# Optimization experiments

Hardware: AMD Instinct MI355X
Metric: run time of the kernel (lower is better)

The kernel has to match this reference:

```python
import jax, jax.numpy as jnp
import numpy as np

POOL_SIZE = 4
MAX_DIM = 256
GRID = MAX_DIM // POOL_SIZE  # 64
NUM_CELLS = GRID * GRID      # 4096
B = 64                        # static max_batch (batch.max()+1 in torch)
N = 1_000_000
C = 64


def setup_inputs() -> dict:
    key = jax.random.key(0)
    k1, k2, k3 = jax.random.split(key, 3)
    x = jax.random.normal(k1, (N, C), dtype=jnp.float32)
    pos = jax.random.randint(k2, (N, 2), 0, MAX_DIM, dtype=jnp.int64)
    batch = jnp.sort(jax.random.randint(k3, (N,), 0, B, dtype=jnp.int64))
    return {"x": x, "pos": pos, "batch": batch}


def reference(x, pos, batch):
    # voxel key: (batch, pos_x//pool, pos_y//pool) -> flat cell index
    qpos = pos[:, :2] // POOL_SIZE                       # [N, 2] int
    idx = batch * NUM_CELLS + qpos[:, 0] * GRID + qpos[:, 1]  # [N]
    num_seg = B * NUM_CELLS
    # scatter_reduce(amax, include_self=False): max over points in each cell
    pooled = jax.ops.segment_max(x, idx, num_segments=num_seg)  # empty -> -inf
    # cells with no points stay zero (output_x initialized to zeros in torch)
    counts = jax.ops.segment_sum(jnp.ones((x.shape[0], 1), x.dtype), idx,
                                 num_segments=num_seg)          # [num_seg, 1]
    pooled = jnp.where(counts > 0, pooled, jnp.zeros((), x.dtype))
    # [B, grid^2, C] -> flatten -> [B, grid^2 * C]
    return pooled.reshape(B, NUM_CELLS * x.shape[1])
```

## Files before the change

kernel.cpp:

```cpp
#include <hip/hip_runtime.h>

#define POOL_SHIFT 2
#define GRID_DIM 64
#define NUM_CELLS 4096
#define NCH 64
#define BATCH 64
#define NSEG (BATCH * NUM_CELLS)
#define SCAN_BLOCKS 1024

__global__ __launch_bounds__(256) void count_kernel(
    const int* __restrict__ pos, const int* __restrict__ batch,
    unsigned int* __restrict__ counts, unsigned int* __restrict__ rank,
    int* __restrict__ cell, int n) {
    int p = blockIdx.x * blockDim.x + threadIdx.x;
    if (p >= n) return;
    int2 pp = ((const int2*)pos)[p];
    int c = batch[p] * NUM_CELLS + (pp.x >> POOL_SHIFT) * GRID_DIM + (pp.y >> POOL_SHIFT);
    cell[p] = c;
    rank[p] = atomicAdd(&counts[c], 1u);
}

__global__ __launch_bounds__(256) void reduce_kernel(
    const unsigned int* __restrict__ counts, unsigned int* __restrict__ blocksum) {
    __shared__ unsigned int s[256];
    int t = threadIdx.x;
    s[t] = counts[blockIdx.x * 256 + t];
    __syncthreads();
    for (int off = 128; off > 0; off >>= 1) {
        if (t < off) s[t] += s[t + off];
        __syncthreads();
    }
    if (t == 0) blocksum[blockIdx.x] = s[0];
}

__global__ __launch_bounds__(1024) void scanblock_kernel(
    const unsigned int* __restrict__ blocksum, unsigned int* __restrict__ blockbase) {
    __shared__ unsigned int s[1024];
    int t = threadIdx.x;
    unsigned int own = blocksum[t];
    s[t] = own;
    __syncthreads();
    for (int off = 1; off < 1024; off <<= 1) {
        unsigned int v = (t >= off) ? s[t - off] : 0u;
        __syncthreads();
        s[t] += v;
        __syncthreads();
    }
    blockbase[t] = s[t] - own;
}

__global__ __launch_bounds__(256) void offsets_kernel(
    const unsigned int* __restrict__ counts, const unsigned int* __restrict__ blockbase,
    unsigned int* __restrict__ offsets, int n) {
    __shared__ unsigned int s[256];
    int t = threadIdx.x, b = blockIdx.x;
    unsigned int own = counts[b * 256 + t];
    s[t] = own;
    __syncthreads();
    for (int off = 1; off < 256; off <<= 1) {
        unsigned int v = (t >= off) ? s[t - off] : 0u;
        __syncthreads();
        s[t] += v;
        __syncthreads();
    }
    unsigned int incl = s[t] + blockbase[b];
    offsets[b * 256 + t] = incl - own;
    if (b == SCAN_BLOCKS - 1 && t == 255) offsets[NSEG] = incl;
}

__global__ __launch_bounds__(256) void reorder_kernel(
    const int* __restrict__ cell, const unsigned int* __restrict__ rank,
    const unsigned int* __restrict__ offsets, unsigned int* __restrict__ order, int n) {
    int p = blockIdx.x * blockDim.x + threadIdx.x;
    if (p >= n) return;
    int c = cell[p];
    order[offsets[c] + rank[p]] = (unsigned int)p;
}

__global__ __launch_bounds__(256) void gather_kernel(
    const float* __restrict__ x, const unsigned int* __restrict__ offsets,
    const unsigned int* __restrict__ order, float* __restrict__ out) {
    int wave = (int)((blockIdx.x * blockDim.x + threadIdx.x) >> 6);
    int lane = threadIdx.x & 63;
    unsigned int s = offsets[wave];
    unsigned int e = offsets[wave + 1];

    size_t obase = (size_t)wave * NCH + lane;
    if (s == e) { out[obase] = 0.0f; return; }

    const float NEG_INF = -__builtin_inff();
    float acc = NEG_INF;

    for (unsigned int base = s; base < e; base += 64) {
        unsigned int rem = e - base;
        unsigned int cnt = rem < 64u ? rem : 64u;
        unsigned int li = lane < cnt ? (unsigned int)lane : cnt - 1u;
        unsigned int myp = order[base + li];

        for (unsigned int j = 0; j < cnt; j += 4) {
            unsigned int m = cnt - j;
            unsigned int p0 = (unsigned int)__shfl((int)myp, (int)j, 64);
            float v0 = x[(size_t)p0 * NCH + lane];
            float v1 = NEG_INF, v2 = NEG_INF, v3 = NEG_INF;
            if (m > 1u) {
                unsigned int p1 = (unsigned int)__shfl((int)myp, (int)(j + 1), 64);
                v1 = x[(size_t)p1 * NCH + lane];
            }
            if (m > 2u) {
                unsigned int p2 = (unsigned int)__shfl((int)myp, (int)(j + 2), 64);
                v2 = x[(size_t)p2 * NCH + lane];
            }
            if (m > 3u) {
                unsigned int p3 = (unsigned int)__shfl((int)myp, (int)(j + 3), 64);
                v3 = x[(size_t)p3 * NCH + lane];
            }
            acc = fmaxf(acc, fmaxf(fmaxf(v0, v1), fmaxf(v2, v3)));
        }
    }
    out[obase] = acc;
}

extern "C" void kernel_launch(void* const* d_in, const int* in_sizes, int n_in,
                              void* d_out, int out_size, void* d_ws, size_t ws_size,
                              hipStream_t stream) {
    const float* x   = (const float*)d_in[0];
    const int* pos   = (const int*)d_in[1];
    const int* batch = (const int*)d_in[2];
    float* out = (float*)d_out;
    int n = in_sizes[2];

    unsigned int* counts    = (unsigned int*)d_ws;
    unsigned int* offsets   = counts + NSEG;
    unsigned int* blocksum  = offsets + NSEG + 1;
    unsigned int* blockbase = blocksum + 1024;
    unsigned int* rank      = blockbase + 1024;
    int*          cell      = (int*)(rank + n);
    unsigned int* order     = (unsigned int*)(cell + n);

    hipMemsetAsync(counts, 0, (size_t)NSEG * sizeof(unsigned int), stream);

    int pblocks = (n + 255) / 256;
    count_kernel<<<pblocks, 256, 0, stream>>>(pos, batch, counts, rank, cell, n);
    reduce_kernel<<<SCAN_BLOCKS, 256, 0, stream>>>(counts, blocksum);
    scanblock_kernel<<<1, 1024, 0, stream>>>(blocksum, blockbase);
    offsets_kernel<<<SCAN_BLOCKS, 256, 0, stream>>>(counts, blockbase, offsets, n);
    reorder_kernel<<<pblocks, 256, 0, stream>>>(cell, rank, offsets, order, n);
    gather_kernel<<<NSEG / 4, 256, 0, stream>>>(x, offsets, order, out);
}
```

Baseline: 445.4 us.

## Pack cell and rank, use wave-shuffle scans, grid-stride loops and nontemporal accesses

Packs the cell index and the per-cell rank into one 32-bit word, so the count and reorder kernels write and read a single array instead of two. Replaces the shared-memory tree reduce and scans with wave-level shuffle reductions and scans. Converts the point and gather kernels to grid-stride loops with fixed grid sizes, and adds nontemporal loads and stores on the streaming x reads and output writes. The packing caps the rank at 14 bits (16384 points per cell), which holds for the expected densities but would silently corrupt results if a cell overflows.

```diff
diff --git a/kernel.cpp b/kernel.cpp
--- a/kernel.cpp
+++ b/kernel.cpp
@@ -7,117 +7,129 @@
 #define BATCH 64
 #define NSEG (BATCH * NUM_CELLS)
 #define SCAN_BLOCKS 1024
+#define RANK_BITS 14
+#define RANK_MASK ((1u << RANK_BITS) - 1u)
 
 __global__ __launch_bounds__(256) void count_kernel(
     const int* __restrict__ pos, const int* __restrict__ batch,
-    unsigned int* __restrict__ counts, unsigned int* __restrict__ rank,
-    int* __restrict__ cell, int n) {
-    int p = blockIdx.x * blockDim.x + threadIdx.x;
-    if (p >= n) return;
-    int2 pp = ((const int2*)pos)[p];
-    int c = batch[p] * NUM_CELLS + (pp.x >> POOL_SHIFT) * GRID_DIM + (pp.y >> POOL_SHIFT);
-    cell[p] = c;
-    rank[p] = atomicAdd(&counts[c], 1u);
+    unsigned int* __restrict__ counts, unsigned int* __restrict__ cellrank, int n) {
+    int stride = gridDim.x * blockDim.x;
+    for (int p = blockIdx.x * blockDim.x + threadIdx.x; p < n; p += stride) {
+        long long t = __builtin_nontemporal_load((const long long*)pos + p);
+        int px = (int)t;
+        int py = (int)(t >> 32);
+        int b  = __builtin_nontemporal_load(&batch[p]);
+        int c  = b * NUM_CELLS + (px >> POOL_SHIFT) * GRID_DIM + (py >> POOL_SHIFT);
+        unsigned int r = atomicAdd(&counts[c], 1u);
+        __builtin_nontemporal_store(((unsigned int)c << RANK_BITS) | r, &cellrank[p]);
+    }
 }
 
 __global__ __launch_bounds__(256) void reduce_kernel(
     const unsigned int* __restrict__ counts, unsigned int* __restrict__ blocksum) {
-    __shared__ unsigned int s[256];
+    __shared__ unsigned int ws[4];
     int t = threadIdx.x;
-    s[t] = counts[blockIdx.x * 256 + t];
+    unsigned int v = counts[blockIdx.x * 256 + t];
+    #pragma unroll
+    for (int off = 1; off < 64; off <<= 1) v += __shfl_xor((int)v, off, 64);
+    if ((t & 63) == 0) ws[t >> 6] = v;
     __syncthreads();
-    for (int off = 128; off > 0; off >>= 1) {
-        if (t < off) s[t] += s[t + off];
-        __syncthreads();
-    }
-    if (t == 0) blocksum[blockIdx.x] = s[0];
+    if (t == 0) blocksum[blockIdx.x] = ws[0] + ws[1] + ws[2] + ws[3];
 }
 
 __global__ __launch_bounds__(1024) void scanblock_kernel(
     const unsigned int* __restrict__ blocksum, unsigned int* __restrict__ blockbase) {
-    __shared__ unsigned int s[1024];
-    int t = threadIdx.x;
+    __shared__ unsigned int wsum[16];
+    int t = threadIdx.x, lane = t & 63, w = t >> 6;
     unsigned int own = blocksum[t];
-    s[t] = own;
+    unsigned int v = own;
+    #pragma unroll
+    for (int off = 1; off < 64; off <<= 1) {
+        unsigned int u = __shfl_up((int)v, off, 64);
+        if (lane >= off) v += u;
+    }
+    if (lane == 63) wsum[w] = v;
     __syncthreads();
-    for (int off = 1; off < 1024; off <<= 1) {
-        unsigned int v = (t >= off) ? s[t - off] : 0u;
-        __syncthreads();
-        s[t] += v;
-        __syncthreads();
-    }
-    blockbase[t] = s[t] - own;
+    unsigned int base = 0;
+    for (int i = 0; i < w; ++i) base += wsum[i];
+    blockbase[t] = v + base - own;
 }
 
 __global__ __launch_bounds__(256) void offsets_kernel(
     const unsigned int* __restrict__ counts, const unsigned int* __restrict__ blockbase,
     unsigned int* __restrict__ offsets, int n) {
-    __shared__ unsigned int s[256];
-    int t = threadIdx.x, b = blockIdx.x;
+    __shared__ unsigned int wsum[4];
+    int t = threadIdx.x, b = blockIdx.x, lane = t & 63, w = t >> 6;
     unsigned int own = counts[b * 256 + t];
-    s[t] = own;
+    unsigned int v = own;
+    #pragma unroll
+    for (int off = 1; off < 64; off <<= 1) {
+        unsigned int u = __shfl_up((int)v, off, 64);
+        if (lane >= off) v += u;
+    }
+    if (lane == 63) wsum[w] = v;
     __syncthreads();
-    for (int off = 1; off < 256; off <<= 1) {
-        unsigned int v = (t >= off) ? s[t - off] : 0u;
-        __syncthreads();
-        s[t] += v;
-        __syncthreads();
-    }
-    unsigned int incl = s[t] + blockbase[b];
+    unsigned int base = blockbase[b];
+    for (int i = 0; i < w; ++i) base += wsum[i];
+    unsigned int incl = v + base;
     offsets[b * 256 + t] = incl - own;
     if (b == SCAN_BLOCKS - 1 && t == 255) offsets[NSEG] = incl;
 }
 
 __global__ __launch_bounds__(256) void reorder_kernel(
-    const int* __restrict__ cell, const unsigned int* __restrict__ rank,
+    const unsigned int* __restrict__ cellrank,
     const unsigned int* __restrict__ offsets, unsigned int* __restrict__ order, int n) {
-    int p = blockIdx.x * blockDim.x + threadIdx.x;
-    if (p >= n) return;
-    int c = cell[p];
-    order[offsets[c] + rank[p]] = (unsigned int)p;
+    int stride = gridDim.x * blockDim.x;
+    for (int p = blockIdx.x * blockDim.x + threadIdx.x; p < n; p += stride) {
+        unsigned int u = __builtin_nontemporal_load(&cellrank[p]);
+        unsigned int c = u >> RANK_BITS;
+        order[offsets[c] + (u & RANK_MASK)] = (unsigned int)p;
+    }
 }
 
 __global__ __launch_bounds__(256) void gather_kernel(
     const float* __restrict__ x, const unsigned int* __restrict__ offsets,
     const unsigned int* __restrict__ order, float* __restrict__ out) {
-    int wave = (int)((blockIdx.x * blockDim.x + threadIdx.x) >> 6);
     int lane = threadIdx.x & 63;
-    unsigned int s = offsets[wave];
-    unsigned int e = offsets[wave + 1];
+    int gw = (int)((blockIdx.x * blockDim.x + threadIdx.x) >> 6);
+    int nw = (int)((gridDim.x * blockDim.x) >> 6);
+    const float NEG_INF = -__builtin_inff();
 
-    size_t obase = (size_t)wave * NCH + lane;
-    if (s == e) { out[obase] = 0.0f; return; }
+    for (int cell = gw; cell < NSEG; cell += nw) {
+        unsigned int s = offsets[cell];
+        unsigned int e = offsets[cell + 1];
+        size_t obase = (size_t)cell * NCH + lane;
+        if (s == e) { __builtin_nontemporal_store(0.0f, &out[obase]); continue; }
 
-    const float NEG_INF = -__builtin_inff();
-    float acc = NEG_INF;
+        float acc = NEG_INF;
+        for (unsigned int base = s; base < e; base += 64) {
+            unsigned int rem = e - base;
+            unsigned int cnt = rem < 64u ? rem : 64u;
+            unsigned int li = (unsigned int)lane < cnt ? (unsigned int)lane : cnt - 1u;
+            unsigned int myp = order[base + li];
 
-    for (unsigned int base = s; base < e; base += 64) {
-        unsigned int rem = e - base;
-        unsigned int cnt = rem < 64u ? rem : 64u;
-        unsigned int li = lane < cnt ? (unsigned int)lane : cnt - 1u;
-        unsigned int myp = order[base + li];
-
-        for (unsigned int j = 0; j < cnt; j += 4) {
-            unsigned int m = cnt - j;
-            unsigned int p0 = (unsigned int)__shfl((int)myp, (int)j, 64);
-            float v0 = x[(size_t)p0 * NCH + lane];
-            float v1 = NEG_INF, v2 = NEG_INF, v3 = NEG_INF;
-            if (m > 1u) {
-                unsigned int p1 = (unsigned int)__shfl((int)myp, (int)(j + 1), 64);
-                v1 = x[(size_t)p1 * NCH + lane];
+            for (unsigned int j = 0; j < cnt; j += 4) {
+                unsigned int m = cnt - j;
+                unsigned int p0 = (unsigned int)__shfl((int)myp, (int)j, 64);
+                float v0 = __builtin_nontemporal_load(&x[(size_t)p0 * NCH + lane]);
+                float v1 = NEG_INF, v2 = NEG_INF, v3 = NEG_INF;
+                if (m > 1u) {
+                    unsigned int p1 = (unsigned int)__shfl((int)myp, (int)(j + 1), 64);
+                    v1 = __builtin_nontemporal_load(&x[(size_t)p1 * NCH + lane]);
+                }
+                if (m > 2u) {
+                    unsigned int p2 = (unsigned int)__shfl((int)myp, (int)(j + 2), 64);
+                    v2 = __builtin_nontemporal_load(&x[(size_t)p2 * NCH + lane]);
+                }
+                if (m > 3u) {
+                    unsigned int p3 = (unsigned int)__shfl((int)myp, (int)(j + 3), 64);
+                    v3 = __builtin_nontemporal_load(&x[(size_t)p3 * NCH + lane]);
+                }
+                acc = fmaxf(acc, fmaxf(fmaxf(v0, v1), fmaxf(v2, v3)));
             }
-            if (m > 2u) {
-                unsigned int p2 = (unsigned int)__shfl((int)myp, (int)(j + 2), 64);
-                v2 = x[(size_t)p2 * NCH + lane];
-            }
-            if (m > 3u) {
-                unsigned int p3 = (unsigned int)__shfl((int)myp, (int)(j + 3), 64);
-                v3 = x[(size_t)p3 * NCH + lane];
-            }
-            acc = fmaxf(acc, fmaxf(fmaxf(v0, v1), fmaxf(v2, v3)));
         }
+        __builtin_nontemporal_store(acc, &out[obase]);
     }
-    out[obase] = acc;
 }
 
 extern "C" void kernel_launch(void* const* d_in, const int* in_sizes, int n_in,
@@ -133,17 +145,15 @@
     unsigned int* offsets   = counts + NSEG;
     unsigned int* blocksum  = offsets + NSEG + 1;
     unsigned int* blockbase = blocksum + 1024;
-    unsigned int* rank      = blockbase + 1024;
-    int*          cell      = (int*)(rank + n);
-    unsigned int* order     = (unsigned int*)(cell + n);
+    unsigned int* cellrank  = blockbase + 1024;
+    unsigned int* order     = cellrank + n;
 
     hipMemsetAsync(counts, 0, (size_t)NSEG * sizeof(unsigned int), stream);
 
-    int pblocks = (n + 255) / 256;
-    count_kernel<<<pblocks, 256, 0, stream>>>(pos, batch, counts, rank, cell, n);
+    count_kernel<<<4096, 256, 0, stream>>>(pos, batch, counts, cellrank, n);
     reduce_kernel<<<SCAN_BLOCKS, 256, 0, stream>>>(counts, blocksum);
     scanblock_kernel<<<1, 1024, 0, stream>>>(blocksum, blockbase);
     offsets_kernel<<<SCAN_BLOCKS, 256, 0, stream>>>(counts, blockbase, offsets, n);
-    reorder_kernel<<<pblocks, 256, 0, stream>>>(cell, rank, offsets, order, n);
-    gather_kernel<<<NSEG / 4, 256, 0, stream>>>(x, offsets, order, out);
+    reorder_kernel<<<4096, 256, 0, stream>>>(cellrank, offsets, order, n);
+    gather_kernel<<<2048, 256, 0, stream>>>(x, offsets, order, out);
 }
```

Result: faster. 431.2 us (-3.2%).

## Replace counting-sort gather with per-batch shared-memory atomicMax pooling

Applied to the files above, without the earlier changes.

Drops the count/scan/reorder/gather pipeline. A small kernel now finds where each batch starts in the sorted batch array, and a single pooling kernel assigns one block to each (batch, 4-channel slice) pair. That block runs atomicMax into a shared-memory grid of 4096 cells x 4 channels, using an order-preserving float-to-int mapping, then writes float4 outputs with empty cells set to zero. This removes the global histogram atomics, the multi-pass scans and the random row gathers. In exchange, pos is reread for every channel slice and there is heavy LDS atomic traffic. It relies on batch being sorted, which the input setup guarantees.

```diff
diff --git a/kernel.cpp b/kernel.cpp
--- a/kernel.cpp
+++ b/kernel.cpp
@@ -5,119 +5,91 @@
 #define NUM_CELLS 4096
 #define NCH 64
 #define BATCH 64
-#define NSEG (BATCH * NUM_CELLS)
-#define SCAN_BLOCKS 1024
+#define QCS 16
+#define SENTINEL ((int)0x80000000)
 
-__global__ __launch_bounds__(256) void count_kernel(
-    const int* __restrict__ pos, const int* __restrict__ batch,
-    unsigned int* __restrict__ counts, unsigned int* __restrict__ rank,
-    int* __restrict__ cell, int n) {
+typedef float vf4 __attribute__((ext_vector_type(4)));
+
+__global__ __launch_bounds__(256) void bounds_kernel(
+    const int* __restrict__ batch, int* __restrict__ bstart, int n) {
     int p = blockIdx.x * blockDim.x + threadIdx.x;
     if (p >= n) return;
-    int2 pp = ((const int2*)pos)[p];
-    int c = batch[p] * NUM_CELLS + (pp.x >> POOL_SHIFT) * GRID_DIM + (pp.y >> POOL_SHIFT);
-    cell[p] = c;
-    rank[p] = atomicAdd(&counts[c], 1u);
+    int b = batch[p];
+    if (p == 0) {
+        for (int i = 0; i <= b; ++i) bstart[i] = 0;
+    } else {
+        int pb = batch[p - 1];
+        for (int i = pb + 1; i <= b; ++i) bstart[i] = p;
+    }
+    if (p == n - 1) {
+        for (int i = b + 1; i <= BATCH; ++i) bstart[i] = n;
+    }
 }
 
-__global__ __launch_bounds__(256) void reduce_kernel(
-    const unsigned int* __restrict__ counts, unsigned int* __restrict__ blocksum) {
-    __shared__ unsigned int s[256];
-    int t = threadIdx.x;
-    s[t] = counts[blockIdx.x * 256 + t];
-    __syncthreads();
-    for (int off = 128; off > 0; off >>= 1) {
-        if (t < off) s[t] += s[t + off];
-        __syncthreads();
-    }
-    if (t == 0) blocksum[blockIdx.x] = s[0];
+__device__ __forceinline__ int fmap(float f) {
+    int i = __float_as_int(f);
+    return i >= 0 ? i : (i ^ 0x7fffffff);
+}
+__device__ __forceinline__ float funmap(int m) {
+    if (m == SENTINEL) return 0.0f;
+    return __int_as_float(m >= 0 ? m : (m ^ 0x7fffffff));
 }
 
-__global__ __launch_bounds__(1024) void scanblock_kernel(
-    const unsigned int* __restrict__ blocksum, unsigned int* __restrict__ blockbase) {
-    __shared__ unsigned int s[1024];
-    int t = threadIdx.x;
-    unsigned int own = blocksum[t];
-    s[t] = own;
-    __syncthreads();
-    for (int off = 1; off < 1024; off <<= 1) {
-        unsigned int v = (t >= off) ? s[t - off] : 0u;
-        __syncthreads();
-        s[t] += v;
-        __syncthreads();
-    }
-    blockbase[t] = s[t] - own;
+__device__ __forceinline__ void accum(int* acc, int2 pp, vf4 v) {
+    int c = ((pp.x >> POOL_SHIFT) << 6) | (pp.y >> POOL_SHIFT);
+    atomicMax(&acc[0 * NUM_CELLS + c], fmap(v.x));
+    atomicMax(&acc[1 * NUM_CELLS + c], fmap(v.y));
+    atomicMax(&acc[2 * NUM_CELLS + c], fmap(v.z));
+    atomicMax(&acc[3 * NUM_CELLS + c], fmap(v.w));
 }
 
-__global__ __launch_bounds__(256) void offsets_kernel(
-    const unsigned int* __restrict__ counts, const unsigned int* __restrict__ blockbase,
-    unsigned int* __restrict__ offsets, int n) {
-    __shared__ unsigned int s[256];
-    int t = threadIdx.x, b = blockIdx.x;
-    unsigned int own = counts[b * 256 + t];
-    s[t] = own;
+__global__ __launch_bounds__(256, 2) void pool_kernel(
+    const float* __restrict__ x, const int* __restrict__ pos,
+    const int* __restrict__ bstart, float* __restrict__ out) {
+    __shared__ int acc[4 * NUM_CELLS];
+    const int L  = (int)blockIdx.x;
+    const int b  = ((L >> 7) << 3) | (L & 7);
+    const int qc = (L >> 3) & 15;
+    const int t  = threadIdx.x;
+
+    for (int i = t; i < 4 * NUM_CELLS; i += 256) acc[i] = SENTINEL;
     __syncthreads();
-    for (int off = 1; off < 256; off <<= 1) {
-        unsigned int v = (t >= off) ? s[t - off] : 0u;
-        __syncthreads();
-        s[t] += v;
-        __syncthreads();
+
+    const int r0 = bstart[b], r1 = bstart[b + 1];
+    const vf4* xq  = (const vf4*)x;
+    const int2* pq = (const int2*)pos;
+
+    int r = r0 + t;
+    for (; r + 768 < r1; r += 1024) {
+        int2 pp0 = pq[r];
+        int2 pp1 = pq[r + 256];
+        int2 pp2 = pq[r + 512];
+        int2 pp3 = pq[r + 768];
+        vf4 v0 = xq[(size_t)r * QCS + qc];
+        vf4 v1 = xq[(size_t)(r + 256) * QCS + qc];
+        vf4 v2 = xq[(size_t)(r + 512) * QCS + qc];
+        vf4 v3 = xq[(size_t)(r + 768) * QCS + qc];
+        accum(acc, pp0, v0);
+        accum(acc, pp1, v1);
+        accum(acc, pp2, v2);
+        accum(acc, pp3, v3);
     }
-    unsigned int incl = s[t] + blockbase[b];
-    offsets[b * 256 + t] = incl - own;
-    if (b == SCAN_BLOCKS - 1 && t == 255) offsets[NSEG] = incl;
-}
+    for (; r < r1; r += 256) {
+        int2 pp = pq[r];
+        vf4 v = xq[(size_t)r * QCS + qc];
+        accum(acc, pp, v);
+    }
+    __syncthreads();
 
-__global__ __launch_bounds__(256) void reorder_kernel(
-    const int* __restrict__ cell, const unsigned int* __restrict__ rank,
-    const unsigned int* __restrict__ offsets, unsigned int* __restrict__ order, int n) {
-    int p = blockIdx.x * blockDim.x + threadIdx.x;
-    if (p >= n) return;
-    int c = cell[p];
-    order[offsets[c] + rank[p]] = (unsigned int)p;
-}
-
-__global__ __launch_bounds__(256) void gather_kernel(
-    const float* __restrict__ x, const unsigned int* __restrict__ offsets,
-    const unsigned int* __restrict__ order, float* __restrict__ out) {
-    int wave = (int)((blockIdx.x * blockDim.x + threadIdx.x) >> 6);
-    int lane = threadIdx.x & 63;
-    unsigned int s = offsets[wave];
-    unsigned int e = offsets[wave + 1];
-
-    size_t obase = (size_t)wave * NCH + lane;
-    if (s == e) { out[obase] = 0.0f; return; }
-
-    const float NEG_INF = -__builtin_inff();
-    float acc = NEG_INF;
-
-    for (unsigned int base = s; base < e; base += 64) {
-        unsigned int rem = e - base;
-        unsigned int cnt = rem < 64u ? rem : 64u;
-        unsigned int li = lane < cnt ? (unsigned int)lane : cnt - 1u;
-        unsigned int myp = order[base + li];
-
-        for (unsigned int j = 0; j < cnt; j += 4) {
-            unsigned int m = cnt - j;
-            unsigned int p0 = (unsigned int)__shfl((int)myp, (int)j, 64);
-            float v0 = x[(size_t)p0 * NCH + lane];
-            float v1 = NEG_INF, v2 = NEG_INF, v3 = NEG_INF;
-            if (m > 1u) {
-                unsigned int p1 = (unsigned int)__shfl((int)myp, (int)(j + 1), 64);
-                v1 = x[(size_t)p1 * NCH + lane];
-            }
-            if (m > 2u) {
-                unsigned int p2 = (unsigned int)__shfl((int)myp, (int)(j + 2), 64);
-                v2 = x[(size_t)p2 * NCH + lane];
-            }
-            if (m > 3u) {
-                unsigned int p3 = (unsigned int)__shfl((int)myp, (int)(j + 3), 64);
-                v3 = x[(size_t)p3 * NCH + lane];
-            }
-            acc = fmaxf(acc, fmaxf(fmaxf(v0, v1), fmaxf(v2, v3)));
-        }
+    const size_t obase = (size_t)b * NUM_CELLS * NCH + (size_t)qc * 4;
+    for (int c = t; c < NUM_CELLS; c += 256) {
+        vf4 o;
+        o.x = funmap(acc[0 * NUM_CELLS + c]);
+        o.y = funmap(acc[1 * NUM_CELLS + c]);
+        o.z = funmap(acc[2 * NUM_CELLS + c]);
+        o.w = funmap(acc[3 * NUM_CELLS + c]);
+        *(vf4*)&out[obase + (size_t)c * NCH] = o;
     }
-    out[obase] = acc;
 }
 
 extern "C" void kernel_launch(void* const* d_in, const int* in_sizes, int n_in,
@@ -129,21 +101,8 @@
     float* out = (float*)d_out;
     int n = in_sizes[2];
 
-    unsigned int* counts    = (unsigned int*)d_ws;
-    unsigned int* offsets   = counts + NSEG;
-    unsigned int* blocksum  = offsets + NSEG + 1;
-    unsigned int* blockbase = blocksum + 1024;
-    unsigned int* rank      = blockbase + 1024;
-    int*          cell      = (int*)(rank + n);
-    unsigned int* order     = (unsigned int*)(cell + n);
+    int* bstart = (int*)d_ws;
 
-    hipMemsetAsync(counts, 0, (size_t)NSEG * sizeof(unsigned int), stream);
-
-    int pblocks = (n + 255) / 256;
-    count_kernel<<<pblocks, 256, 0, stream>>>(pos, batch, counts, rank, cell, n);
-    reduce_kernel<<<SCAN_BLOCKS, 256, 0, stream>>>(counts, blocksum);
-    scanblock_kernel<<<1, 1024, 0, stream>>>(blocksum, blockbase);
-    offsets_kernel<<<SCAN_BLOCKS, 256, 0, stream>>>(counts, blockbase, offsets, n);
-    reorder_kernel<<<pblocks, 256, 0, stream>>>(cell, rank, offsets, order, n);
-    gather_kernel<<<NSEG / 4, 256, 0, stream>>>(x, offsets, order, out);
+    bounds_kernel<<<(n + 255) / 256, 256, 0, stream>>>(batch, bstart, n);
+    pool_kernel<<<BATCH * QCS, 256, 0, stream>>>(x, pos, bstart, out);
 }
```

New measurement: 408.9 us. 1.09x faster.
